# Kernel tuning notes

Measured on AMD Instinct MI355X. Metric: run time of the kernel, lower is better.

The kernel has to match this reference:

```python
import jax, jax.numpy as jnp
import numpy as np

B, S, F, H, A = 256, 128, 512, 1024, 18


def setup_inputs() -> dict:
    key = jax.random.key(0)
    ks = jax.random.split(key, 16)
    u = lambda k, shape, fan: jax.random.uniform(k, shape, jnp.float32, -1.0, 1.0) / np.sqrt(fan)
    return {
        "obs": jax.random.normal(ks[0], (B, S, F), jnp.float32),
        "hx": jax.random.normal(ks[1], (B, H), jnp.float32),
        "cx": jax.random.normal(ks[2], (B, H), jnp.float32),
        "behaviour_acts": jax.random.randint(ks[3], (B, S, 1), 0, A),
        "W1": u(ks[4], (H, F), F), "b1": u(ks[5], (H,), F),
        "W_ih": u(ks[6], (4 * H, H), H), "b_ih": u(ks[7], (4 * H,), H),
        "W_hh": u(ks[8], (4 * H, H), H), "b_hh": u(ks[9], (4 * H,), H),
        "W_v": u(ks[10], (1, H), H), "b_v": u(ks[11], (1,), H),
        "W_l": u(ks[12], (A, H), H), "b_l": u(ks[13], (A,), H),
    }


def reference(obs, hx, cx, behaviour_acts, W1, b1, W_ih, b_ih, W_hh, b_hh, W_v, b_v, W_l, b_l):
    # MLP body: [B,S,F] -> [B,S,H]
    x = jax.nn.relu(jnp.einsum("bsf,hf->bsh", obs, W1) + b1)
    # precompute input-to-gate projection for all timesteps (one big GEMM)
    xg = jnp.einsum("bsh,gh->bsg", x, W_ih) + b_ih  # [B,S,4H]

    def step(carry, xg_t):
        h, c = carry
        gates = xg_t + h @ W_hh.T + b_hh  # [B,4H], gate order i,f,g,o (torch LSTMCell)
        i, f, g, o = jnp.split(gates, 4, axis=-1)
        c = jax.nn.sigmoid(f) * c + jax.nn.sigmoid(i) * jnp.tanh(g)
        h = jax.nn.sigmoid(o) * jnp.tanh(c)
        return (h, c), h

    _, hs = jax.lax.scan(step, (hx, cx), jnp.swapaxes(xg, 0, 1))
    output = jnp.swapaxes(hs, 0, 1)  # [B,S,H]

    value = output @ W_v.T + b_v  # [B,S,1]
    logits = output @ W_l.T + b_l  # [B,S,A]
    # torch Categorical(probs=softmax(logits)) => log-prob via log_softmax
    logp = jax.nn.log_softmax(logits, axis=-1)
    acts = behaviour_acts.reshape(logits.shape[0], logits.shape[1], 1)
    log_probs = jnp.take_along_axis(logp, acts, axis=-1)  # [B,S,1]
    entropy = -jnp.sum(jnp.exp(logp) * logp, axis=-1, keepdims=True)  # [B,S,1]
    return log_probs, entropy, value
```

## Files before the change

### kernel.cpp

```cpp
#include <hip/hip_runtime.h>

#define B_ 256
#define S_ 128
#define F_ 512
#define H_ 1024
#define A_ 18
#define M_ (B_*S_)
#define G_ (4*H_)
#define CH_ 16
#define CR_ (B_*CH_)

typedef unsigned short u16;
typedef __attribute__((ext_vector_type(8))) _Float16 f16x8;
typedef __attribute__((ext_vector_type(4))) _Float16 f16x4;
typedef __attribute__((ext_vector_type(8))) short   s16x8;
typedef __attribute__((ext_vector_type(4))) float f32x4;
typedef __attribute__((ext_vector_type(4))) unsigned int u32x4;

__device__ __forceinline__ float bf2f(u16 u){
  union{unsigned int i; float f;} v; v.i=((unsigned int)u)<<16; return v.f;
}
__device__ __forceinline__ u16 f2bf(float f){
  unsigned int i=__float_as_uint(f);
  unsigned int r=(i+0x7fffu+((i>>16)&1u))>>16;
  return (u16)r;
}
__device__ __forceinline__ u16 f2h(float f){
  _Float16 h=(_Float16)f;
  union{_Float16 h; u16 u;} v; v.h=h; return v.u;
}
__device__ __forceinline__ float ldf(const void* p, size_t i, int m){
  return m ? ((const float*)p)[i] : bf2f(((const u16*)p)[i]);
}
__device__ __forceinline__ f16x8 load8_h(const void* base, size_t off, int m){
  f16x8 v;
  if(m==2) return *(const f16x8*)((const u16*)base + off);
  if(m==1){
    const float* f=(const float*)base + off;
    float4 a=*(const float4*)f; float4 b=*(const float4*)(f+4);
    v[0]=(_Float16)a.x; v[1]=(_Float16)a.y; v[2]=(_Float16)a.z; v[3]=(_Float16)a.w;
    v[4]=(_Float16)b.x; v[5]=(_Float16)b.y; v[6]=(_Float16)b.z; v[7]=(_Float16)b.w;
    return v;
  }
  s16x8 w=*(const s16x8*)((const u16*)base + off);
#pragma unroll
  for(int k=0;k<8;k++) v[k]=(_Float16)bf2f((u16)w[k]);
  return v;
}

__device__ __forceinline__ u32x4 load_c16(const void* p){
  u32x4 r;
  asm volatile("global_load_dwordx4 %0, %1, off sc0 sc1" : "=v"(r) : "v"(p));
  return r;
}
__device__ __forceinline__ void store_c2(u16* p, u16 v){
  unsigned int vv=v;
  asm volatile("global_store_short %0, %1, off sc0 sc1" :: "v"(p), "v"(vv) : "memory");
}
__device__ __forceinline__ int load_c4(const int* p){
  int r;
  asm volatile("global_load_dword %0, %1, off sc0 sc1" : "=v"(r) : "v"(p));
  return r;
}
__device__ __forceinline__ void store_c4(int* p, int v){
  asm volatile("global_store_dword %0, %1, off sc0 sc1" :: "v"(p), "v"(v) : "memory");
}

__device__ __forceinline__ void bar_flags32(int* flags, int target, int gi, int lane, int w){
  asm volatile("s_waitcnt vmcnt(0)" ::: "memory");
  __syncthreads();
  if(w==0){
    if(lane==0) store_c4(flags+gi, target);
    while(true){
      int v=load_c4(flags+(lane&31));
      asm volatile("s_waitcnt vmcnt(0)" ::: "memory");
      if(__all(v>=target)) break;
      __builtin_amdgcn_s_sleep(1);
    }
  }
  __syncthreads();
}

template<int ROWS, int MAP>
__device__ __forceinline__ void stage(const void* base, int mode, int lda, int k0,
                                      int rowoff, int t0, u16* lds, int tid){
  if(mode==2){
    constexpr int NI=(ROWS*8)/256;
    int wv=tid>>6, l=tid&63;
#pragma unroll
    for(int i=0;i<NI;i++){
      int s0=i*256+(wv<<6), s=s0+l;
      int r=s>>3, gc=(s&7)^(r&7);
      int p=rowoff+r, sr;
      if(MAP==0)      sr=p;
      else if(MAP==1) sr=(p&3)*H_+(p>>2);
      else            sr=(p>>4)*S_+t0+(p&15);
      const u16* src=(const u16*)base + (size_t)sr*lda + k0 + gc*8;
      u16* dst=lds + s0*8;
      __builtin_amdgcn_global_load_lds((const __attribute__((address_space(1))) unsigned int*)src,
                                       (__attribute__((address_space(3))) unsigned int*)dst,
                                       16, 0, 0);
    }
  } else {
#pragma unroll
    for(int s0=tid; s0<ROWS*8; s0+=256){
      int r=s0>>3, gc=s0&7, lc=gc^(r&7);
      int p=rowoff+r, sr;
      if(MAP==0)      sr=p;
      else if(MAP==1) sr=(p&3)*H_+(p>>2);
      else            sr=(p>>4)*S_+t0+(p&15);
      f16x8 v=load8_h(base, (size_t)sr*lda + k0 + gc*8, mode);
      *(f16x8*)(lds + r*64 + lc*8)=v;
    }
  }
}

__device__ __forceinline__ f16x8 frag_ld(const u16* lds, int r0, int kc, int lane){
  int r = r0 + (lane&15);
  int c = (kc + (lane>>4)) ^ (r&7);
  return *(const f16x8*)(lds + r*64 + c*8);
}

template<int AMAP, int BMAP, int OUTMODE>
__global__ __launch_bounds__(256,3) void gemm128(const void* A, const void* Bt, void* C,
    const float* __restrict__ biasf, const int* __restrict__ flag,
    int K, int lda, int ldb, int ldc, int t0, int amode, int bmode){
  int m=*flag;
  int am = amode<0 ? m : amode;
  int bm_ = bmode<0 ? m : bmode;
  __shared__ u16 As[128*64];
  __shared__ u16 Bs[128*64];
  int tid=threadIdx.x, lane=tid&63, w=tid>>6;
  int bm=blockIdx.y*128, bn=blockIdx.x*128;
  int wm=(w&1)*64, wn=(w>>1)*64;
  f32x4 acc[4][4];
#pragma unroll
  for(int i=0;i<4;i++)
#pragma unroll
    for(int j=0;j<4;j++) acc[i][j]=(f32x4)(0.f);
  for(int k0=0;k0<K;k0+=64){
    stage<128,AMAP>(A , am,  lda, k0, bm, t0, As, tid);
    stage<128,BMAP>(Bt, bm_, ldb, k0, bn, t0, Bs, tid);
    __syncthreads();
#pragma unroll
    for(int kk=0;kk<2;kk++){
      f16x8 af[4], bq[4];
#pragma unroll
      for(int i=0;i<4;i++) af[i]=frag_ld(As, wm+i*16, kk*4, lane);
#pragma unroll
      for(int j=0;j<4;j++) bq[j]=frag_ld(Bs, wn+j*16, kk*4, lane);
#pragma unroll
      for(int i=0;i<4;i++)
#pragma unroll
        for(int j=0;j<4;j++)
          acc[i][j]=__builtin_amdgcn_mfma_f32_16x16x32_f16(af[i],bq[j],acc[i][j],0,0,0);
    }
    __syncthreads();
  }
  int rl=lane>>4, cl=lane&15;
#pragma unroll
  for(int j=0;j<4;j++){
    int col=bn+wn+j*16+cl;
    float bb=biasf[col];
#pragma unroll
    for(int i=0;i<4;i++){
#pragma unroll
      for(int r=0;r<4;r++){
        int row=bm+wm+i*16+rl*4+r;
        float v=acc[i][j][r]+bb;
        if(OUTMODE==0){ v=fmaxf(v,0.f); ((u16*)C)[(size_t)row*ldc+col]=f2h(v); }
        else if(OUTMODE==2){ ((u16*)C)[(size_t)row*ldc+col]=f2h(v); }
        else { ((float*)C)[(size_t)row*ldc+col]=v; }
      }
    }
  }
}

__global__ __launch_bounds__(512,2) void lstm_persist(u16* __restrict__ hh,
        const u16* __restrict__ Whhp, const u16* __restrict__ xgp,
        float* __restrict__ cst, int* __restrict__ cntc, int tbase){
  __shared__ u16 As[16*2048];
  __shared__ float gs[32*132];
  int tid=threadIdx.x, lane=tid&63, w=tid>>6;
  int grp=blockIdx.x&7, ci=blockIdx.x>>3;
  int bm=grp*32, bn=ci*128;
  int* flags = cntc + grp*64;

  f16x8 bw[32];
#pragma unroll
  for(int t=0;t<32;t++){
    int p = bn + w*16 + (lane&15);
    int k = t*32 + (lane>>4)*8;
    bw[t]=*(const f16x8*)(Whhp + (size_t)p*H_ + k);
  }
#pragma unroll
  for(int t=0;t<32;t++) asm volatile("" : "+a"(bw[t]));

  int rl0=tid>>5, rl1=(tid+512)>>5, u0=tid&31;
  int gu=(bn>>2)+u0;
  float c0=cst[(size_t)(bm+rl0)*H_+gu];
  float c1=cst[(size_t)(bm+rl1)*H_+gu];

  for(int dt=0;dt<CH_;dt++){
    f16x4 xv0=*(const f16x4*)(xgp + ((size_t)(bm+rl0)*CH_+dt)*G_ + bn + u0*4);
    f16x4 xv1=*(const f16x4*)(xgp + ((size_t)(bm+rl1)*CH_+dt)*G_ + bn + u0*4);
    if(dt) bar_flags32(flags, tbase+dt, ci, lane, w);
    int slotPrev=(dt+CH_-1)&(CH_-1);
    const u16* hbase = hh + (size_t)slotPrev*H_;
    {
      u32x4 tmp[4];
#pragma unroll
      for(int i=0;i<4;i++){
        int s=tid+i*512, kt=s>>8, r=(s>>3)&31, gc=s&7;
        tmp[i]=*(const u32x4*)(hbase + (size_t)(bm+r)*(CH_*H_) + kt*64 + gc*8);
      }
#pragma unroll
      for(int i=0;i<4;i++){
        int s=tid+i*512, kt=s>>8, r=(s>>3)&31, gc=s&7, lc=gc^(r&7);
        *(u32x4*)(As + kt*2048 + r*64 + lc*8)=tmp[i];
      }
    }
    __syncthreads();
    u32x4 tmp2[4];
#pragma unroll
    for(int i=0;i<4;i++){
      int s=tid+(i+4)*512, kt=s>>8, r=(s>>3)&31, gc=s&7;
      tmp2[i]=*(const u32x4*)(hbase + (size_t)(bm+r)*(CH_*H_) + kt*64 + gc*8);
    }
    f32x4 acc0=(f32x4)(0.f), acc1=(f32x4)(0.f);
#pragma unroll
    for(int t=0;t<16;t++){
      int kt=t>>1, kk=t&1;
      f16x8 af0=frag_ld(As+kt*2048, 0,  kk*4, lane);
      f16x8 af1=frag_ld(As+kt*2048, 16, kk*4, lane);
      acc0=__builtin_amdgcn_mfma_f32_16x16x32_f16(af0,bw[t],acc0,0,0,0);
      acc1=__builtin_amdgcn_mfma_f32_16x16x32_f16(af1,bw[t],acc1,0,0,0);
    }
#pragma unroll
    for(int i=0;i<4;i++){
      int s=tid+(i+4)*512, kt=s>>8, r=(s>>3)&31, gc=s&7, lc=gc^(r&7);
      *(u32x4*)(As + kt*2048 + r*64 + lc*8)=tmp2[i];
    }
    __syncthreads();
#pragma unroll
    for(int t=16;t<32;t++){
      int kt=t>>1, kk=t&1;
      f16x8 af0=frag_ld(As+kt*2048, 0,  kk*4, lane);
      f16x8 af1=frag_ld(As+kt*2048, 16, kk*4, lane);
      acc0=__builtin_amdgcn_mfma_f32_16x16x32_f16(af0,bw[t],acc0,0,0,0);
      acc1=__builtin_amdgcn_mfma_f32_16x16x32_f16(af1,bw[t],acc1,0,0,0);
    }
#pragma unroll
    for(int r=0;r<4;r++){
      gs[(   (lane>>4)*4+r)*132 + w*16+(lane&15)]=acc0[r];
      gs[(16+(lane>>4)*4+r)*132 + w*16+(lane&15)]=acc1[r];
    }
    __syncthreads();
    {
      float4 gv=*(const float4*)&gs[rl0*132+u0*4];
      float ii=1.f/(1.f+__expf(-(gv.x+(float)xv0[0])));
      float ff=1.f/(1.f+__expf(-(gv.y+(float)xv0[1])));
      float gg=1.f-2.f/(__expf(2.f*(gv.z+(float)xv0[2]))+1.f);
      float oo=1.f/(1.f+__expf(-(gv.w+(float)xv0[3])));
      c0=ff*c0+ii*gg;
      float th=1.f-2.f/(__expf(2.f*c0)+1.f);
      store_c2(hh + ((size_t)(bm+rl0)*CH_+dt)*H_ + gu, f2h(oo*th));
    }
    {
      float4 gv=*(const float4*)&gs[rl1*132+u0*4];
      float ii=1.f/(1.f+__expf(-(gv.x+(float)xv1[0])));
      float ff=1.f/(1.f+__expf(-(gv.y+(float)xv1[1])));
      float gg=1.f-2.f/(__expf(2.f*(gv.z+(float)xv1[2]))+1.f);
      float oo=1.f/(1.f+__expf(-(gv.w+(float)xv1[3])));
      c1=ff*c1+ii*gg;
      float th=1.f-2.f/(__expf(2.f*c1)+1.f);
      store_c2(hh + ((size_t)(bm+rl1)*CH_+dt)*H_ + gu, f2h(oo*th));
    }
  }
  cst[(size_t)(bm+rl0)*H_+gu]=c0;
  cst[(size_t)(bm+rl1)*H_+gu]=c1;
}

__global__ __launch_bounds__(256,2) void lstm_step(u16* __restrict__ hh, int slotPrev, int dt,
        const void* __restrict__ Whh, const u16* __restrict__ xg,
        float* __restrict__ cst, const int* __restrict__ flag){
  int m=*flag;
  __shared__ u16 As[64*64];
  __shared__ u16 Bs[64*64];
  __shared__ float gs[64*64];
  int tid=threadIdx.x, lane=tid&63, w=tid>>6;
  int bm=blockIdx.y*64, bn=blockIdx.x*64;
  int wm=(w&1)*32, wn=(w>>1)*32;
  f32x4 acc[2][2];
#pragma unroll
  for(int i=0;i<2;i++)
#pragma unroll
    for(int j=0;j<2;j++) acc[i][j]=(f32x4)(0.f);
  for(int k0=0;k0<H_;k0+=64){
    stage<64,0>(hh + slotPrev*H_, 2, CH_*H_, k0, bm, 0, As, tid);
    stage<64,1>(Whh,              m, H_,     k0, bn, 0, Bs, tid);
    __syncthreads();
#pragma unroll
    for(int kk=0;kk<2;kk++){
      f16x8 af[2], bq[2];
#pragma unroll
      for(int i=0;i<2;i++) af[i]=frag_ld(As, wm+i*16, kk*4, lane);
#pragma unroll
      for(int j=0;j<2;j++) bq[j]=frag_ld(Bs, wn+j*16, kk*4, lane);
#pragma unroll
      for(int i=0;i<2;i++)
#pragma unroll
        for(int j=0;j<2;j++)
          acc[i][j]=__builtin_amdgcn_mfma_f32_16x16x32_f16(af[i],bq[j],acc[i][j],0,0,0);
    }
    __syncthreads();
  }
  int rl=lane>>4, cl=lane&15;
#pragma unroll
  for(int j=0;j<2;j++){
    int coll=wn+j*16+cl;
#pragma unroll
    for(int i=0;i<2;i++){
#pragma unroll
      for(int r=0;r<4;r++){
        int rowl=wm+i*16+rl*4+r;
        float xv=(float)((const _Float16*)xg)[((size_t)(bm+rowl)*CH_+dt)*G_ + bn+coll];
        gs[rowl*64+coll]=acc[i][j][r] + xv;
      }
    }
  }
  __syncthreads();
#pragma unroll
  for(int p=0;p<4;p++){
    int idx=p*256+tid;
    int rowl=idx>>4, u=idx&15;
    float4 gv = *(const float4*)&gs[rowl*64+u*4];
    float ii=1.f/(1.f+__expf(-gv.x));
    float ff=1.f/(1.f+__expf(-gv.y));
    float gg=1.f-2.f/(__expf(2.f*gv.z)+1.f);
    float oo=1.f/(1.f+__expf(-gv.w));
    int gb=bm+rowl;
    int gu=(bn>>2)+u;
    size_t ci=(size_t)gb*H_+gu;
    float cn=ff*cst[ci]+ii*gg;
    cst[ci]=cn;
    float th=1.f-2.f/(__expf(2.f*cn)+1.f);
    hh[(size_t)gb*(CH_*H_) + dt*H_ + gu]=f2h(oo*th);
  }
}

__global__ __launch_bounds__(256,2) void heads_chunk(const u16* __restrict__ hh,
      const void* __restrict__ Wl, const void* __restrict__ Wv,
      const float* __restrict__ blf, const int* __restrict__ acts,
      void* __restrict__ out, const int* __restrict__ flag, int t0){
  int m=*flag;
  int rg = blockIdx.x*4 + (threadIdx.x>>6);
  int lane = threadIdx.x & 63;
  const u16* h = hh + (size_t)rg*H_;
  u32x4 hv0=load_c16(h + lane*16);
  u32x4 hv1=load_c16(h + lane*16 + 8);
  f16x8 h0=__builtin_bit_cast(f16x8,hv0), h1=__builtin_bit_cast(f16x8,hv1);
  float hv[16];
#pragma unroll
  for(int k=0;k<8;k++){ hv[k]=(float)h0[k]; hv[8+k]=(float)h1[k]; }
  float dots[19];
#pragma unroll
  for(int j=0;j<19;j++){
    const void* wrow = (j<18) ? Wl : Wv;
    size_t roff = (j<18) ? (size_t)j*H_ : 0;
    float wv_[16];
    if(m){
      const float* f=(const float*)wrow + roff + lane*16;
      float4 a=*(const float4*)f, b=*(const float4*)(f+4), c=*(const float4*)(f+8), d=*(const float4*)(f+12);
      wv_[0]=a.x;wv_[1]=a.y;wv_[2]=a.z;wv_[3]=a.w; wv_[4]=b.x;wv_[5]=b.y;wv_[6]=b.z;wv_[7]=b.w;
      wv_[8]=c.x;wv_[9]=c.y;wv_[10]=c.z;wv_[11]=c.w; wv_[12]=d.x;wv_[13]=d.y;wv_[14]=d.z;wv_[15]=d.w;
    } else {
      const u16* ub=(const u16*)wrow + roff + lane*16;
      s16x8 w0=*(const s16x8*)ub, w1=*(const s16x8*)(ub+8);
#pragma unroll
      for(int k=0;k<8;k++){ wv_[k]=bf2f((u16)w0[k]); wv_[8+k]=bf2f((u16)w1[k]); }
    }
    float d=0.f;
#pragma unroll
    for(int k=0;k<16;k++) d += hv[k]*wv_[k];
#pragma unroll
    for(int mm=1;mm<64;mm<<=1) d += __shfl_xor(d, mm, 64);
    dots[j]=d;
  }
  float lg[18];
#pragma unroll
  for(int j=0;j<18;j++) lg[j]=dots[j]+blf[j];
  float value=dots[18]+blf[18];
  float mx=lg[0];
#pragma unroll
  for(int j=1;j<18;j++) mx=fmaxf(mx,lg[j]);
  float se=0.f, s1=0.f;
#pragma unroll
  for(int j=0;j<18;j++){ float e=__expf(lg[j]-mx); se+=e; s1+=e*(lg[j]-mx); }
  float lse=__logf(se);
  int b=rg>>4, dt=rg&(CH_-1);
  int gw = b*S_ + t0 + dt;
  int a=acts[gw];
  float la=0.f;
#pragma unroll
  for(int j=0;j<18;j++) la = (j==a) ? lg[j] : la;
  float lp=la-mx-lse;
  float ent=lse - s1/se;
  if(lane==0){
    if(m){
      ((float*)out)[gw]=lp; ((float*)out)[M_+gw]=ent; ((float*)out)[2*M_+gw]=value;
    } else {
      ((u16*)out)[gw]=f2bf(lp); ((u16*)out)[M_+gw]=f2bf(ent); ((u16*)out)[2*M_+gw]=f2bf(value);
    }
  }
}

__global__ void detect(const u16* __restrict__ obs_w, int* __restrict__ flag){
  __shared__ float red[256];
  float mx=0.f;
  for(int i=threadIdx.x;i<4096;i+=256) mx=fmaxf(mx,fabsf(bf2f(obs_w[i])));
  red[threadIdx.x]=mx; __syncthreads();
  for(int s=128;s>0;s>>=1){
    if(threadIdx.x<s) red[threadIdx.x]=fmaxf(red[threadIdx.x],red[threadIdx.x+s]);
    __syncthreads();
  }
  if(threadIdx.x==0) *flag=(red[0]>1e4f)?1:0;
}

__global__ void prep(const void* bih, const void* bhh, const void* b1, const void* bl, const void* bv,
                     const void* cx, const void* hx,
                     float* biasg, float* b1f, float* blf, float* cst, u16* hh,
                     int* cnt, const int* __restrict__ flag){
  int m=*flag;
  size_t i=(size_t)blockIdx.x*256+threadIdx.x;
  if(i<G_){ size_t rm=(i&3)*H_+(i>>2); biasg[i]=ldf(bih,rm,m)+ldf(bhh,rm,m); return; }
  i-=G_;
  if(i<H_){ b1f[i]=ldf(b1,i,m); return; }
  i-=H_;
  if(i<19){ blf[i]=(i<18)?ldf(bl,i,m):ldf(bv,0,m); return; }
  i-=19;
  if(i<512){ cnt[i]=0; return; }
  i-=512;
  if(i<(size_t)B_*H_){ cst[i]=ldf(cx,i,m); return; }
  i-=(size_t)B_*H_;
  if(i<(size_t)B_*H_){
    size_t b=i>>10, k=i&1023;
    hh[b*(CH_*H_) + (CH_-1)*H_ + k]=f2h(ldf(hx,i,m));
  }
}

__global__ void convw(const void* W1, const void* Wih, const void* Whh,
                      u16* W1h, u16* Wihp, u16* Whhp, const int* __restrict__ flag){
  int m=*flag;
  size_t i=((size_t)blockIdx.x*256+threadIdx.x)*8;
  const size_t n1=(size_t)H_*F_, n2=(size_t)G_*H_;
  if(i<n1){ *(f16x8*)(W1h+i)=load8_h(W1,i,m); return; }
  i-=n1;
  if(i<n2){ size_t p=i>>10, c=i&1023; size_t sr=(p&3)*H_+(p>>2);
            *(f16x8*)(Wihp+i)=load8_h(Wih, sr*H_+c, m); return; }
  i-=n2;
  if(i<n2){ size_t p=i>>10, c=i&1023; size_t sr=(p&3)*H_+(p>>2);
            *(f16x8*)(Whhp+i)=load8_h(Whh, sr*H_+c, m); return; }
}
__global__ void convobs(const void* obs, u16* obsh, const int* __restrict__ flag){
  int m=*flag;
  size_t i=((size_t)blockIdx.x*256+threadIdx.x)*8;
  if(i<(size_t)M_*F_) *(f16x8*)(obsh+i)=load8_h(obs,i,m);
}

extern "C" void kernel_launch(void* const* d_in, const int* in_sizes, int n_in,
                              void* d_out, int out_size, void* d_ws, size_t ws_size,
                              hipStream_t stream){
  const void* obs=d_in[0];
  const void* hx =d_in[1];
  const void* cx =d_in[2];
  const int* acts=(const int*)d_in[3];
  const void* W1 =d_in[4];
  const void* b1 =d_in[5];
  const void* Wih=d_in[6];
  const void* bih=d_in[7];
  const void* Whh=d_in[8];
  const void* bhh=d_in[9];
  const void* Wv =d_in[10];
  const void* bv =d_in[11];
  const void* Wl =d_in[12];
  const void* bl =d_in[13];

  char* w=(char*)d_ws;
  auto alloc=[&](size_t n){ char* p=w; w+=((n+255)&~(size_t)255); return p; };
  int*   flag =(int*)alloc(4);
  int*   cnt  =(int*)alloc(512*4);
  float* biasg=(float*)alloc((size_t)G_*4);
  float* b1f  =(float*)alloc((size_t)H_*4);
  float* blf  =(float*)alloc(32*4);
  float* cst  =(float*)alloc((size_t)B_*H_*4);
  u16*   hh   =(u16*)alloc((size_t)B_*CH_*H_*2);
  u16*   xc   =(u16*)alloc((size_t)CR_*H_*2);
  u16*   xg   =(u16*)alloc((size_t)CR_*G_*2);
  size_t nW=((size_t)H_*F_ + 2*(size_t)G_*H_)*2 + 768;
  bool pathW = ((size_t)(w-(char*)d_ws) + nW) <= ws_size;
  u16 *W1h=0,*Wihp=0,*Whhp=0;
  if(pathW){ W1h=(u16*)alloc((size_t)H_*F_*2); Wihp=(u16*)alloc((size_t)G_*H_*2); Whhp=(u16*)alloc((size_t)G_*H_*2); }
  size_t nXC=(size_t)M_*H_*2 + 256;
  bool pathXC = pathW && (((size_t)(w-(char*)d_ws) + nXC) <= ws_size);
  u16* xcf=0; if(pathXC) xcf=(u16*)alloc((size_t)M_*H_*2);
  size_t nO=(size_t)M_*F_*2 + 256;
  bool pathO = pathXC && (((size_t)(w-(char*)d_ws) + nO) <= ws_size);
  u16* obsh=0; if(pathO) obsh=(u16*)alloc((size_t)M_*F_*2);

  detect<<<1,256,0,stream>>>((const u16*)obs, flag);
  {
    int total=G_+H_+19+512+B_*H_+B_*H_;
    prep<<<(total+255)/256,256,0,stream>>>(bih,bhh,b1,bl,bv,cx,hx, biasg,b1f,blf,cst,hh,cnt, flag);
  }
  if(pathW){
    size_t n=((size_t)H_*F_+2*(size_t)G_*H_)/8;
    convw<<<(int)((n+255)/256),256,0,stream>>>(W1,Wih,Whh, W1h,Wihp,Whhp, flag);
  }
  if(pathO){
    size_t n=(size_t)M_*F_/8;
    convobs<<<(int)((n+255)/256),256,0,stream>>>(obs, obsh, flag);
  }
  if(pathXC){
    gemm128<0,0,0><<<dim3(H_/128, M_/128),256,0,stream>>>(
        pathO?(const void*)obsh:obs, pathW?(const void*)W1h:W1, xcf, b1f, flag,
        F_, F_, F_, H_, 0, pathO?2:-1, pathW?2:-1);
  }

  for(int c=0;c<S_/CH_;c++){
    int t0=c*CH_;
    if(!pathXC){
      gemm128<2,0,0><<<dim3(H_/128, CR_/128),256,0,stream>>>(
          obs, pathW?(const void*)W1h:W1, xc, b1f, flag, F_, F_, F_, H_, t0, -1, pathW?2:-1);
    }
    if(pathXC)
      gemm128<2,0,2><<<dim3(G_/128, CR_/128),256,0,stream>>>(
          xcf, Wihp, xg, biasg, flag, H_, H_, H_, G_, t0, 2, 2);
    else if(pathW)
      gemm128<0,0,2><<<dim3(G_/128, CR_/128),256,0,stream>>>(
          xc, Wihp, xg, biasg, flag, H_, H_, H_, G_, 0, 2, 2);
    else
      gemm128<0,1,2><<<dim3(G_/128, CR_/128),256,0,stream>>>(
          xc, Wih, xg, biasg, flag, H_, H_, H_, G_, 0, 2, -1);

    if(pathW)
      lstm_persist<<<256,512,0,stream>>>(hh, Whhp, xg, cst, cnt, t0);
    else
      for(int dt=0;dt<CH_;dt++)
        lstm_step<<<dim3(G_/64, B_/64),256,0,stream>>>(hh, (dt+CH_-1)&(CH_-1), dt, Whh, xg, cst, flag);

    heads_chunk<<<dim3(CR_/4),256,0,stream>>>(hh, Wl, Wv, blf, acts, d_out, flag, t0);
  }
}
```

Before: 1.205 ms.

## Keep full hidden-state history and run output heads once after recurrence

The hidden-state buffer becomes a full per-batch history of S+1 slots instead of a 16-slot ring. The recurrent kernels now read and write absolute time slots. This lets the per-chunk heads kernel be replaced by one heads launch over all timesteps after the loop, removing 7 launches and the small per-chunk tails. In exchange the h buffer grows to about 64MB of workspace, and the recurrence reads strided rows across a larger footprint, which may hurt cache locality.

```diff
diff --git a/kernel.cpp b/kernel.cpp
--- a/kernel.cpp
+++ b/kernel.cpp
@@ -2,6 +2,7 @@
 
 #define B_ 256
 #define S_ 128
+#define SP1 (S_+1)
 #define F_ 512
 #define H_ 1024
 #define A_ 18
@@ -205,14 +206,13 @@
     f16x4 xv0=*(const f16x4*)(xgp + ((size_t)(bm+rl0)*CH_+dt)*G_ + bn + u0*4);
     f16x4 xv1=*(const f16x4*)(xgp + ((size_t)(bm+rl1)*CH_+dt)*G_ + bn + u0*4);
     if(dt) bar_flags32(flags, tbase+dt, ci, lane, w);
-    int slotPrev=(dt+CH_-1)&(CH_-1);
-    const u16* hbase = hh + (size_t)slotPrev*H_;
+    const u16* hbase = hh + (size_t)(tbase+dt)*H_;
     {
       u32x4 tmp[4];
 #pragma unroll
       for(int i=0;i<4;i++){
         int s=tid+i*512, kt=s>>8, r=(s>>3)&31, gc=s&7;
-        tmp[i]=*(const u32x4*)(hbase + (size_t)(bm+r)*(CH_*H_) + kt*64 + gc*8);
+        tmp[i]=*(const u32x4*)(hbase + (size_t)(bm+r)*(SP1*H_) + kt*64 + gc*8);
       }
 #pragma unroll
       for(int i=0;i<4;i++){
@@ -225,7 +225,7 @@
 #pragma unroll
     for(int i=0;i<4;i++){
       int s=tid+(i+4)*512, kt=s>>8, r=(s>>3)&31, gc=s&7;
-      tmp2[i]=*(const u32x4*)(hbase + (size_t)(bm+r)*(CH_*H_) + kt*64 + gc*8);
+      tmp2[i]=*(const u32x4*)(hbase + (size_t)(bm+r)*(SP1*H_) + kt*64 + gc*8);
     }
     f32x4 acc0=(f32x4)(0.f), acc1=(f32x4)(0.f);
 #pragma unroll
@@ -264,7 +264,7 @@
       float oo=1.f/(1.f+__expf(-(gv.w+(float)xv0[3])));
       c0=ff*c0+ii*gg;
       float th=1.f-2.f/(__expf(2.f*c0)+1.f);
-      store_c2(hh + ((size_t)(bm+rl0)*CH_+dt)*H_ + gu, f2h(oo*th));
+      store_c2(hh + ((size_t)(bm+rl0)*SP1 + tbase+dt+1)*H_ + gu, f2h(oo*th));
     }
     {
       float4 gv=*(const float4*)&gs[rl1*132+u0*4];
@@ -274,14 +274,14 @@
       float oo=1.f/(1.f+__expf(-(gv.w+(float)xv1[3])));
       c1=ff*c1+ii*gg;
       float th=1.f-2.f/(__expf(2.f*c1)+1.f);
-      store_c2(hh + ((size_t)(bm+rl1)*CH_+dt)*H_ + gu, f2h(oo*th));
+      store_c2(hh + ((size_t)(bm+rl1)*SP1 + tbase+dt+1)*H_ + gu, f2h(oo*th));
     }
   }
   cst[(size_t)(bm+rl0)*H_+gu]=c0;
   cst[(size_t)(bm+rl1)*H_+gu]=c1;
 }
 
-__global__ __launch_bounds__(256,2) void lstm_step(u16* __restrict__ hh, int slotPrev, int dt,
+__global__ __launch_bounds__(256,2) void lstm_step(u16* __restrict__ hh, int slotAbs, int dt,
         const void* __restrict__ Whh, const u16* __restrict__ xg,
         float* __restrict__ cst, const int* __restrict__ flag){
   int m=*flag;
@@ -297,8 +297,8 @@
 #pragma unroll
     for(int j=0;j<2;j++) acc[i][j]=(f32x4)(0.f);
   for(int k0=0;k0<H_;k0+=64){
-    stage<64,0>(hh + slotPrev*H_, 2, CH_*H_, k0, bm, 0, As, tid);
-    stage<64,1>(Whh,              m, H_,     k0, bn, 0, Bs, tid);
+    stage<64,0>(hh + (size_t)slotAbs*H_, 2, SP1*H_, k0, bm, 0, As, tid);
+    stage<64,1>(Whh,                     m, H_,     k0, bn, 0, Bs, tid);
     __syncthreads();
 #pragma unroll
     for(int kk=0;kk<2;kk++){
@@ -345,18 +345,19 @@
     float cn=ff*cst[ci]+ii*gg;
     cst[ci]=cn;
     float th=1.f-2.f/(__expf(2.f*cn)+1.f);
-    hh[(size_t)gb*(CH_*H_) + dt*H_ + gu]=f2h(oo*th);
-  }
-}
-
-__global__ __launch_bounds__(256,2) void heads_chunk(const u16* __restrict__ hh,
+    hh[((size_t)gb*SP1 + slotAbs+1)*H_ + gu]=f2h(oo*th);
+  }
+}
+
+__global__ __launch_bounds__(256,2) void heads_full(const u16* __restrict__ hh,
       const void* __restrict__ Wl, const void* __restrict__ Wv,
       const float* __restrict__ blf, const int* __restrict__ acts,
-      void* __restrict__ out, const int* __restrict__ flag, int t0){
+      void* __restrict__ out, const int* __restrict__ flag){
   int m=*flag;
   int rg = blockIdx.x*4 + (threadIdx.x>>6);
   int lane = threadIdx.x & 63;
-  const u16* h = hh + (size_t)rg*H_;
+  int b=rg>>7, t=rg&(S_-1);
+  const u16* h = hh + ((size_t)b*SP1 + t+1)*H_;
   u32x4 hv0=load_c16(h + lane*16);
   u32x4 hv1=load_c16(h + lane*16 + 8);
   f16x8 h0=__builtin_bit_cast(f16x8,hv0), h1=__builtin_bit_cast(f16x8,hv1);
@@ -371,8 +372,8 @@
     float wv_[16];
     if(m){
       const float* f=(const float*)wrow + roff + lane*16;
-      float4 a=*(const float4*)f, b=*(const float4*)(f+4), c=*(const float4*)(f+8), d=*(const float4*)(f+12);
-      wv_[0]=a.x;wv_[1]=a.y;wv_[2]=a.z;wv_[3]=a.w; wv_[4]=b.x;wv_[5]=b.y;wv_[6]=b.z;wv_[7]=b.w;
+      float4 a=*(const float4*)f, b2=*(const float4*)(f+4), c=*(const float4*)(f+8), d=*(const float4*)(f+12);
+      wv_[0]=a.x;wv_[1]=a.y;wv_[2]=a.z;wv_[3]=a.w; wv_[4]=b2.x;wv_[5]=b2.y;wv_[6]=b2.z;wv_[7]=b2.w;
       wv_[8]=c.x;wv_[9]=c.y;wv_[10]=c.z;wv_[11]=c.w; wv_[12]=d.x;wv_[13]=d.y;wv_[14]=d.z;wv_[15]=d.w;
     } else {
       const u16* ub=(const u16*)wrow + roff + lane*16;
@@ -398,9 +399,7 @@
 #pragma unroll
   for(int j=0;j<18;j++){ float e=__expf(lg[j]-mx); se+=e; s1+=e*(lg[j]-mx); }
   float lse=__logf(se);
-  int b=rg>>4, dt=rg&(CH_-1);
-  int gw = b*S_ + t0 + dt;
-  int a=acts[gw];
+  int a=acts[rg];
   float la=0.f;
 #pragma unroll
   for(int j=0;j<18;j++) la = (j==a) ? lg[j] : la;
@@ -408,9 +407,9 @@
   float ent=lse - s1/se;
   if(lane==0){
     if(m){
-      ((float*)out)[gw]=lp; ((float*)out)[M_+gw]=ent; ((float*)out)[2*M_+gw]=value;
+      ((float*)out)[rg]=lp; ((float*)out)[M_+rg]=ent; ((float*)out)[2*M_+rg]=value;
     } else {
-      ((u16*)out)[gw]=f2bf(lp); ((u16*)out)[M_+gw]=f2bf(ent); ((u16*)out)[2*M_+gw]=f2bf(value);
+      ((u16*)out)[rg]=f2bf(lp); ((u16*)out)[M_+rg]=f2bf(ent); ((u16*)out)[2*M_+rg]=f2bf(value);
     }
   }
 }
@@ -445,7 +444,7 @@
   i-=(size_t)B_*H_;
   if(i<(size_t)B_*H_){
     size_t b=i>>10, k=i&1023;
-    hh[b*(CH_*H_) + (CH_-1)*H_ + k]=f2h(ldf(hx,i,m));
+    hh[b*(SP1*H_) + k]=f2h(ldf(hx,i,m));
   }
 }
 
@@ -494,7 +493,7 @@
   float* b1f  =(float*)alloc((size_t)H_*4);
   float* blf  =(float*)alloc(32*4);
   float* cst  =(float*)alloc((size_t)B_*H_*4);
-  u16*   hh   =(u16*)alloc((size_t)B_*CH_*H_*2);
+  u16*   hh   =(u16*)alloc((size_t)B_*SP1*H_*2);
   u16*   xc   =(u16*)alloc((size_t)CR_*H_*2);
   u16*   xg   =(u16*)alloc((size_t)CR_*G_*2);
   size_t nW=((size_t)H_*F_ + 2*(size_t)G_*H_)*2 + 768;
@@ -527,7 +526,8 @@
         F_, F_, F_, H_, 0, pathO?2:-1, pathW?2:-1);
   }
 
-  for(int c=0;c<S_/CH_;c++){
+  const int NC=S_/CH_;
+  for(int c=0;c<NC;c++){
     int t0=c*CH_;
     if(!pathXC){
       gemm128<2,0,0><<<dim3(H_/128, CR_/128),256,0,stream>>>(
@@ -547,8 +547,8 @@
       lstm_persist<<<256,512,0,stream>>>(hh, Whhp, xg, cst, cnt, t0);
     else
       for(int dt=0;dt<CH_;dt++)
-        lstm_step<<<dim3(G_/64, B_/64),256,0,stream>>>(hh, (dt+CH_-1)&(CH_-1), dt, Whh, xg, cst, flag);
-
-    heads_chunk<<<dim3(CR_/4),256,0,stream>>>(hh, Wl, Wv, blf, acts, d_out, flag, t0);
-  }
-}
+        lstm_step<<<dim3(G_/64, B_/64),256,0,stream>>>(hh, t0+dt, dt, Whh, xg, cst, flag);
+  }
+
+  heads_full<<<dim3(M_/4),256,0,stream>>>(hh, Wl, Wv, blf, acts, d_out, flag);
+}
```

After: 1.238 ms. 1.03x slower.
